# Kernel optimization log

Measured on AMD Instinct MI355X. Metric: run time of the kernel, lower is better.

The kernel has to match this reference:

```python
import jax, jax.numpy as jnp
import numpy as np

N, D, OUT, K = 1_000_000, 128, 128, 10
B2 = 4096            # final batch of nodes
B1 = B2 * K          # depth-1 frontier size


def setup_inputs() -> dict:
    key = jax.random.key(0)
    k1, k2, k3, k4, k5, k6, k7 = jax.random.split(key, 7)
    raw_features = jax.random.normal(k1, (N, D), dtype=jnp.float32)
    # SageLayer weights: [out, 2*in] (gcn=False => concat(self, agg))
    W1 = jax.random.normal(k2, (OUT, 2 * D), dtype=jnp.float32) * 0.05
    W2 = jax.random.normal(k3, (OUT, 2 * OUT), dtype=jnp.float32) * 0.05
    # depth-1 frontier node ids and their K sampled neighbors (global ids)
    nodes1 = jax.random.randint(k4, (B1,), 0, N)
    neigh1 = jax.random.randint(k5, (B1, K), 0, N)
    # batch nodes remapped to local indices into the depth-1 hidden table
    nodes2 = jax.random.randint(k6, (B2,), 0, B1)
    neigh2 = jax.random.randint(k7, (B2, K), 0, B1)
    return {"raw_features": raw_features, "W1": W1, "W2": W2,
            "nodes1": nodes1, "neigh1": neigh1,
            "nodes2": nodes2, "neigh2": neigh2}


def sage_layer(self_feats, agg_feats, W):
    # relu(concat(self, agg) @ W^T), matching SageLayer with gcn=False
    combined = jnp.concatenate([self_feats, agg_feats], axis=1)
    return jax.nn.relu(combined @ W.T)


def reference(raw_features, W1, W2, nodes1, neigh1, nodes2, neigh2):
    # Layer 1: mean-aggregate sampled neighbor raw features (gather + mean
    # replaces the dense mask.mm mean in the original).
    agg1 = jnp.mean(raw_features[neigh1], axis=1)      # [B1, D]
    h1 = sage_layer(raw_features[nodes1], agg1, W1)    # [B1, OUT]
    # Layer 2: neighbors indexed locally into the layer-1 hidden table
    agg2 = jnp.mean(h1[neigh2], axis=1)                # [B2, OUT]
    h2 = sage_layer(h1[nodes2], agg2, W2)              # [B2, OUT]
    return h2
```

## Files before the change

kernel.cpp:

```cpp
#include <hip/hip_runtime.h>


typedef __attribute__((ext_vector_type(8))) short  short8;
typedef __attribute__((ext_vector_type(8))) __bf16 bf16x8;
typedef __attribute__((ext_vector_type(4))) float  f32x4;

#define K_NEIGH 10
#define NB      32
#define PITCH   264

__device__ inline float b2f(short s) {
    union { unsigned int u; float f; } c;
    c.u = ((unsigned int)(unsigned short)s) << 16;
    return c.f;
}
__device__ inline short f2b(float f) {
    union { float f; unsigned int u; } c; c.f = f;
    unsigned int u = c.u;
    return (short)((u + 0x7fffu + ((u >> 16) & 1u)) >> 16);
}
__device__ inline unsigned int pack2(float lo, float hi) {
    return (unsigned int)(unsigned short)f2b(lo)
         | ((unsigned int)(unsigned short)f2b(hi) << 16);
}
__device__ inline bf16x8 as_bf16x8(short8 s) {
    union { short8 s; bf16x8 b; } c; c.s = s; return c.b;
}

__global__ void detect_f32(const unsigned short* __restrict__ w, int* __restrict__ flag) {
    const int lane = threadIdx.x;
    unsigned int e = ((unsigned int)w[2 * lane] >> 7) & 0xFFu;
    unsigned long long m = __ballot(e >= 132u);
    if (lane == 0) *flag = (m != 0ull) ? 1 : 0;
}

__launch_bounds__(256, 8)
__global__ void gather_agg(const void* __restrict__ table,
                           const int*  __restrict__ nodes,
                           const int*  __restrict__ neigh,
                           short*      __restrict__ comb,
                           const int*  __restrict__ flag,
                           const int table_by_flag)
{
    const int t    = threadIdx.x;
    const int lane = t & 63;
    const int node = blockIdx.x * 4 + (t >> 6);
    const bool t32 = table_by_flag && *flag;

    const int self_id = nodes[node];
    int nid[K_NEIGH];
#pragma unroll
    for (int k = 0; k < K_NEIGH; ++k) nid[k] = neigh[node * K_NEIGH + k];

    unsigned int sp;
    float a0 = 0.f, a1 = 0.f;

    if (t32) {
        const float* base = (const float*)table;
        float2 self = *(const float2*)(base + (long)self_id * 128 + lane * 2);
        float2 v[K_NEIGH];
#pragma unroll
        for (int k = 0; k < K_NEIGH; ++k)
            v[k] = *(const float2*)(base + (long)nid[k] * 128 + lane * 2);
#pragma unroll
        for (int k = 0; k < K_NEIGH; ++k) { a0 += v[k].x; a1 += v[k].y; }
        sp = pack2(self.x, self.y);
    } else {
        const short* base = (const short*)table;
        sp = *(const unsigned int*)(base + (long)self_id * 128 + lane * 2);
        unsigned int v[K_NEIGH];
#pragma unroll
        for (int k = 0; k < K_NEIGH; ++k)
            v[k] = *(const unsigned int*)(base + (long)nid[k] * 128 + lane * 2);
#pragma unroll
        for (int k = 0; k < K_NEIGH; ++k) {
            a0 += b2f((short)(v[k] & 0xFFFFu));
            a1 += b2f((short)(v[k] >> 16));
        }
    }
    unsigned int gp = pack2(a0 * 0.1f, a1 * 0.1f);
    unsigned int* crow = (unsigned int*)(comb + (long)node * 256);
    crow[lane]      = sp;
    crow[64 + lane] = gp;
}

__launch_bounds__(256, 2)
__global__ void gemm_combined(const short* __restrict__ comb,
                              const void* __restrict__ Wv,
                              void*       __restrict__ outv,
                              const int*  __restrict__ flag,
                              const int out_by_flag)
{
    __shared__ __align__(16) short lds[NB * PITCH];
    const int t    = threadIdx.x;
    const int blk  = blockIdx.x;
    const int lane = t & 63;
    const int wave = t >> 6;
    const int n15  = lane & 15;
    const int q    = lane >> 4;
    const int f32in = *flag;
    const bool o32 = out_by_flag && f32in;

    short8 bfrag[2][8];
    if (!f32in) {
        const short* W = (const short*)Wv;
#pragma unroll
        for (int ot = 0; ot < 2; ++ot) {
            const int o = wave * 32 + ot * 16 + n15;
#pragma unroll
            for (int fk = 0; fk < 8; ++fk)
                bfrag[ot][fk] = *(const short8*)(W + o * 256 + fk * 32 + q * 8);
        }
    } else {
        const float* W = (const float*)Wv;
#pragma unroll
        for (int ot = 0; ot < 2; ++ot) {
            const int o = wave * 32 + ot * 16 + n15;
#pragma unroll
            for (int fk = 0; fk < 8; ++fk) {
                const float* p = W + o * 256 + fk * 32 + q * 8;
                f32x4 v0 = *(const f32x4*)p;
                f32x4 v1 = *(const f32x4*)(p + 4);
                short8 s;
#pragma unroll
                for (int i = 0; i < 4; ++i) { s[i] = f2b(v0[i]); s[4 + i] = f2b(v1[i]); }
                bfrag[ot][fk] = s;
            }
        }
    }

    {
        const int m   = t >> 3;
        const int col = (t & 7) * 32;
        const short* src = comb + (long)blk * (NB * 256) + m * 256 + col;
        short8 x0 = *(const short8*)(src);
        short8 x1 = *(const short8*)(src + 8);
        short8 x2 = *(const short8*)(src + 16);
        short8 x3 = *(const short8*)(src + 24);
        short* dst = lds + m * PITCH + col;
        *(short8*)(dst)      = x0;
        *(short8*)(dst + 8)  = x1;
        *(short8*)(dst + 16) = x2;
        *(short8*)(dst + 24) = x3;
    }
    __syncthreads();

    f32x4 acc[2][2] = {};
#pragma unroll
    for (int mb = 0; mb < 2; ++mb) {
        const short* arow = lds + (mb * 16 + n15) * PITCH + q * 8;
        short8 af[8];
#pragma unroll
        for (int fk = 0; fk < 8; ++fk) af[fk] = *(const short8*)(arow + fk * 32);
#pragma unroll
        for (int ot = 0; ot < 2; ++ot)
#pragma unroll
            for (int fk = 0; fk < 8; ++fk)
                acc[mb][ot] = __builtin_amdgcn_mfma_f32_16x16x32_bf16(
                    as_bf16x8(af[fk]), as_bf16x8(bfrag[ot][fk]), acc[mb][ot], 0, 0, 0);
    }

#pragma unroll
    for (int mb = 0; mb < 2; ++mb)
#pragma unroll
        for (int ot = 0; ot < 2; ++ot) {
            const int col = wave * 32 + ot * 16 + n15;
#pragma unroll
            for (int r = 0; r < 4; ++r) {
                const long row = blk * NB + mb * 16 + q * 4 + r;
                float v = acc[mb][ot][r];
                v = v > 0.f ? v : 0.f;
                if (!o32) ((short*)outv)[row * 128 + col] = f2b(v);
                else      ((float*)outv)[row * 128 + col] = v;
            }
        }
}

__launch_bounds__(256, 2)
__global__ void sage_layer(const void* __restrict__ table,
                           const void* __restrict__ Wv,
                           const int*  __restrict__ nodes,
                           const int*  __restrict__ neigh,
                           void*       __restrict__ outv,
                           const int*  __restrict__ flag,
                           const int table_by_flag, const int out_by_flag)
{
    __shared__ __align__(16) short lds[NB * PITCH];
    const int t    = threadIdx.x;
    const int blk  = blockIdx.x;
    const int lane = t & 63;
    const int wave = t >> 6;
    const int n15  = lane & 15;
    const int q    = lane >> 4;
    const int f32in = *flag;
    const bool t32 = table_by_flag && f32in;
    const bool o32 = out_by_flag && f32in;

    short8 bfrag[2][8];
    if (!f32in) {
        const short* W = (const short*)Wv;
#pragma unroll
        for (int ot = 0; ot < 2; ++ot) {
            const int o = wave * 32 + ot * 16 + n15;
#pragma unroll
            for (int fk = 0; fk < 8; ++fk)
                bfrag[ot][fk] = *(const short8*)(W + o * 256 + fk * 32 + q * 8);
        }
    } else {
        const float* W = (const float*)Wv;
#pragma unroll
        for (int ot = 0; ot < 2; ++ot) {
            const int o = wave * 32 + ot * 16 + n15;
#pragma unroll
            for (int fk = 0; fk < 8; ++fk) {
                const float* p = W + o * 256 + fk * 32 + q * 8;
                f32x4 v0 = *(const f32x4*)p;
                f32x4 v1 = *(const f32x4*)(p + 4);
                short8 s;
#pragma unroll
                for (int i = 0; i < 4; ++i) { s[i] = f2b(v0[i]); s[4 + i] = f2b(v1[i]); }
                bfrag[ot][fk] = s;
            }
        }
    }

    {
        const int m    = t >> 3;
        const int part = t & 7;
        const int gi   = blk * NB + m;
        const int self_id = nodes[gi];
        int nidv[K_NEIGH];
#pragma unroll
        for (int k = 0; k < K_NEIGH; ++k) nidv[k] = neigh[gi * K_NEIGH + k];
        short8 s0, s1;
        float a[16];
#pragma unroll
        for (int i = 0; i < 16; ++i) a[i] = 0.f;

        if (!t32) {
            const short* srow = (const short*)table + (long)self_id * 128 + part * 16;
            s0 = *(const short8*)(srow);
            s1 = *(const short8*)(srow + 8);
#pragma unroll
            for (int k = 0; k < K_NEIGH; ++k) {
                const short* nrow = (const short*)table + (long)nidv[k] * 128 + part * 16;
                short8 v0 = *(const short8*)(nrow);
                short8 v1 = *(const short8*)(nrow + 8);
#pragma unroll
                for (int i = 0; i < 8; ++i) { a[i] += b2f(v0[i]); a[8 + i] += b2f(v1[i]); }
            }
        } else {
            const float* srow = (const float*)table + (long)self_id * 128 + part * 16;
            f32x4 u0 = *(const f32x4*)(srow);
            f32x4 u1 = *(const f32x4*)(srow + 4);
            f32x4 u2 = *(const f32x4*)(srow + 8);
            f32x4 u3 = *(const f32x4*)(srow + 12);
#pragma unroll
            for (int i = 0; i < 4; ++i) {
                s0[i] = f2b(u0[i]); s0[4 + i] = f2b(u1[i]);
                s1[i] = f2b(u2[i]); s1[4 + i] = f2b(u3[i]);
            }
#pragma unroll
            for (int k = 0; k < K_NEIGH; ++k) {
                const float* nrow = (const float*)table + (long)nidv[k] * 128 + part * 16;
                f32x4 v0 = *(const f32x4*)(nrow);
                f32x4 v1 = *(const f32x4*)(nrow + 4);
                f32x4 v2 = *(const f32x4*)(nrow + 8);
                f32x4 v3 = *(const f32x4*)(nrow + 12);
#pragma unroll
                for (int i = 0; i < 4; ++i) {
                    a[i] += v0[i]; a[4 + i] += v1[i]; a[8 + i] += v2[i]; a[12 + i] += v3[i];
                }
            }
        }
        short8 g0, g1;
#pragma unroll
        for (int i = 0; i < 8; ++i) { g0[i] = f2b(a[i] * 0.1f); g1[i] = f2b(a[8 + i] * 0.1f); }
        short* dst = lds + m * PITCH + part * 16;
        *(short8*)(dst)       = s0;
        *(short8*)(dst + 8)   = s1;
        *(short8*)(dst + 128) = g0;
        *(short8*)(dst + 136) = g1;
    }
    __syncthreads();

    f32x4 acc[2][2] = {};
#pragma unroll
    for (int mb = 0; mb < 2; ++mb) {
        const short* arow = lds + (mb * 16 + n15) * PITCH + q * 8;
        short8 af[8];
#pragma unroll
        for (int fk = 0; fk < 8; ++fk) af[fk] = *(const short8*)(arow + fk * 32);
#pragma unroll
        for (int ot = 0; ot < 2; ++ot)
#pragma unroll
            for (int fk = 0; fk < 8; ++fk)
                acc[mb][ot] = __builtin_amdgcn_mfma_f32_16x16x32_bf16(
                    as_bf16x8(af[fk]), as_bf16x8(bfrag[ot][fk]), acc[mb][ot], 0, 0, 0);
    }

#pragma unroll
    for (int mb = 0; mb < 2; ++mb)
#pragma unroll
        for (int ot = 0; ot < 2; ++ot) {
            const int col = wave * 32 + ot * 16 + n15;
#pragma unroll
            for (int r = 0; r < 4; ++r) {
                const long row = blk * NB + mb * 16 + q * 4 + r;
                float v = acc[mb][ot][r];
                v = v > 0.f ? v : 0.f;
                if (!o32) ((short*)outv)[row * 128 + col] = f2b(v);
                else      ((float*)outv)[row * 128 + col] = v;
            }
        }
}

extern "C" void kernel_launch(void* const* d_in, const int* in_sizes, int n_in,
                              void* d_out, int out_size, void* d_ws, size_t ws_size,
                              hipStream_t stream) {
    const void* raw    = d_in[0];
    const void* W1     = d_in[1];
    const void* W2     = d_in[2];
    const int*  nodes1 = (const int*)d_in[3];
    const int*  neigh1 = (const int*)d_in[4];
    const int*  nodes2 = (const int*)d_in[5];
    const int*  neigh2 = (const int*)d_in[6];

    int*   flag = (int*)d_ws;
    short* h1   = (short*)((char*)d_ws + 256);
    short* comb = (short*)((char*)d_ws + 256 + 10485760);

    const int B1 = in_sizes[3];
    const int B2 = in_sizes[5];

    detect_f32<<<1, 64, 0, stream>>>((const unsigned short*)W1, flag);
    gather_agg<<<B1 / 4, 256, 0, stream>>>(raw, nodes1, neigh1, comb, flag,
                                           1);
    gemm_combined<<<B1 / NB, 256, 0, stream>>>(comb, W1, h1, flag, 0);
    sage_layer<<<B2 / NB, 256, 0, stream>>>(h1, W2, nodes2, neigh2, d_out, flag,
                                            0, 1);
}
```

Baseline: 630.8 us.

## Bucket-sort layer-1 row references before gathering raw feature rows

Adds a counting-sort pipeline (histogram, scan, scatter) that orders all self and neighbor row references by 128-row bucket. Rows are then gathered in sorted order into a staging buffer, and a separate mean kernel reads them back by position. The aim is to turn random HBM row reads of the 512 MB feature table into locality-friendly accesses. The cost is several extra launches, atomics, and writing then re-reading about 90 MB of staged rows. The old path is kept as a fallback when the workspace is too small.

```diff
diff --git a/kernel.cpp b/kernel.cpp
--- a/kernel.cpp
+++ b/kernel.cpp
@@ -8,6 +8,7 @@
 #define K_NEIGH 10
 #define NB      32
 #define PITCH   264
+#define NBUCKET 8192
 
 __device__ inline float b2f(short s) {
     union { unsigned int u; float f; } c;
@@ -32,6 +33,151 @@
     unsigned int e = ((unsigned int)w[2 * lane] >> 7) & 0xFFu;
     unsigned long long m = __ballot(e >= 132u);
     if (lane == 0) *flag = (m != 0ull) ? 1 : 0;
+}
+
+
+__global__ void hist_refs(const int* __restrict__ nodes,
+                          const int* __restrict__ neigh,
+                          const int B1, const int total,
+                          int* __restrict__ hist)
+{
+    const int r = blockIdx.x * 256 + threadIdx.x;
+    if (r < total) {
+        const int id = (r < B1) ? nodes[r] : neigh[r - B1];
+        atomicAdd(&hist[id >> 7], 1);
+    }
+}
+
+__global__ void scan8k(const int* __restrict__ hist, int* __restrict__ cursor)
+{
+    __shared__ int part[1024];
+    const int tid = threadIdx.x;
+    int v[8], run[8];
+    int s = 0;
+#pragma unroll
+    for (int i = 0; i < 8; ++i) {
+        v[i] = hist[tid * 8 + i];
+        run[i] = s;
+        s += v[i];
+    }
+    part[tid] = s;
+    __syncthreads();
+    for (int off = 1; off < 1024; off <<= 1) {
+        int x = (tid >= off) ? part[tid - off] : 0;
+        __syncthreads();
+        part[tid] += x;
+        __syncthreads();
+    }
+    const int base = part[tid] - s;
+#pragma unroll
+    for (int i = 0; i < 8; ++i)
+        cursor[tid * 8 + i] = base + run[i];
+}
+
+__global__ void scatter_refs(const int* __restrict__ nodes,
+                             const int* __restrict__ neigh,
+                             const int B1, const int total,
+                             int* __restrict__ cursor,
+                             int* __restrict__ sorted_id,
+                             int* __restrict__ pos_of)
+{
+    const int r = blockIdx.x * 256 + threadIdx.x;
+    if (r < total) {
+        const int id = (r < B1) ? nodes[r] : neigh[r - B1];
+        const int p  = atomicAdd(&cursor[id >> 7], 1);
+        sorted_id[p] = id;
+        pos_of[r]    = p;
+    }
+}
+
+__launch_bounds__(256, 8)
+__global__ void gather_rows(const void* __restrict__ table,
+                            const int*  __restrict__ sorted_id,
+                            void*       __restrict__ gath,
+                            const int*  __restrict__ flag,
+                            const int total, const int table_by_flag)
+{
+    const int  t    = threadIdx.x;
+    const int  lane = t & 63;
+    const long p0   = ((long)blockIdx.x * 4 + (t >> 6)) * 4;
+    const bool t32  = table_by_flag && *flag;
+
+    int id[4];
+#pragma unroll
+    for (int j = 0; j < 4; ++j) {
+        const long p = p0 + j;
+        id[j] = (p < total) ? sorted_id[p] : 0;
+    }
+    if (t32) {
+        const float2* src = (const float2*)table;
+        float2*       dst = (float2*)gath;
+        float2 v[4];
+#pragma unroll
+        for (int j = 0; j < 4; ++j) v[j] = src[(long)id[j] * 64 + lane];
+#pragma unroll
+        for (int j = 0; j < 4; ++j) {
+            const long p = p0 + j;
+            if (p < total) dst[p * 64 + lane] = v[j];
+        }
+    } else {
+        const unsigned int* src = (const unsigned int*)table;
+        unsigned int*       dst = (unsigned int*)gath;
+        unsigned int v[4];
+#pragma unroll
+        for (int j = 0; j < 4; ++j) v[j] = src[(long)id[j] * 64 + lane];
+#pragma unroll
+        for (int j = 0; j < 4; ++j) {
+            const long p = p0 + j;
+            if (p < total) dst[p * 64 + lane] = v[j];
+        }
+    }
+}
+
+__launch_bounds__(256, 8)
+__global__ void mean_refs(const void* __restrict__ gath,
+                          const int*  __restrict__ pos_of,
+                          short*      __restrict__ comb,
+                          const int*  __restrict__ flag,
+                          const int B1, const int table_by_flag)
+{
+    const int t    = threadIdx.x;
+    const int lane = t & 63;
+    const int n    = blockIdx.x * 4 + (t >> 6);
+    if (n >= B1) return;
+    const bool t32 = table_by_flag && *flag;
+
+    const int sp_i = pos_of[n];
+    int np[K_NEIGH];
+#pragma unroll
+    for (int k = 0; k < K_NEIGH; ++k) np[k] = pos_of[B1 + n * K_NEIGH + k];
+
+    unsigned int sp;
+    float a0 = 0.f, a1 = 0.f;
+    if (t32) {
+        const float2* g = (const float2*)gath;
+        float2 self = g[(long)sp_i * 64 + lane];
+        float2 v[K_NEIGH];
+#pragma unroll
+        for (int k = 0; k < K_NEIGH; ++k) v[k] = g[(long)np[k] * 64 + lane];
+#pragma unroll
+        for (int k = 0; k < K_NEIGH; ++k) { a0 += v[k].x; a1 += v[k].y; }
+        sp = pack2(self.x, self.y);
+    } else {
+        const unsigned int* g = (const unsigned int*)gath;
+        sp = g[(long)sp_i * 64 + lane];
+        unsigned int v[K_NEIGH];
+#pragma unroll
+        for (int k = 0; k < K_NEIGH; ++k) v[k] = g[(long)np[k] * 64 + lane];
+#pragma unroll
+        for (int k = 0; k < K_NEIGH; ++k) {
+            a0 += b2f((short)(v[k] & 0xFFFFu));
+            a1 += b2f((short)(v[k] >> 16));
+        }
+    }
+    const unsigned int gp = pack2(a0 * 0.1f, a1 * 0.1f);
+    unsigned int* crow = (unsigned int*)(comb + (long)n * 256);
+    crow[lane]      = sp;
+    crow[64 + lane] = gp;
 }
 
 __launch_bounds__(256, 8)
@@ -54,7 +200,6 @@
 
     unsigned int sp;
     float a0 = 0.f, a1 = 0.f;
-
     if (t32) {
         const float* base = (const float*)table;
         float2 self = *(const float2*)(base + (long)self_id * 128 + lane * 2);
@@ -326,16 +471,47 @@
     const int*  nodes2 = (const int*)d_in[5];
     const int*  neigh2 = (const int*)d_in[6];
 
-    int*   flag = (int*)d_ws;
-    short* h1   = (short*)((char*)d_ws + 256);
-    short* comb = (short*)((char*)d_ws + 256 + 10485760);
-
-    const int B1 = in_sizes[3];
-    const int B2 = in_sizes[5];
+    const int B1    = in_sizes[3];
+    const int B2    = in_sizes[5];
+    const int total = B1 * (1 + K_NEIGH);
+
+    char* ws = (char*)d_ws;
+    int*   flag      = (int*)ws;
+    size_t o_h1      = 256;
+    size_t o_comb    = o_h1   + (size_t)B1 * 128 * 2;
+    size_t o_hist    = o_comb + (size_t)B1 * 256 * 2;
+    size_t o_cursor  = o_hist   + (size_t)NBUCKET * 4;
+    size_t o_sid     = o_cursor + (size_t)NBUCKET * 4;
+    size_t o_pos     = o_sid    + (size_t)total * 4;
+    size_t o_gath    = o_pos    + (size_t)total * 4;
+    size_t need      = o_gath   + (size_t)total * 512;
+
+    short* h1        = (short*)(ws + o_h1);
+    short* comb      = (short*)(ws + o_comb);
+    int*   hist      = (int*)(ws + o_hist);
+    int*   cursor    = (int*)(ws + o_cursor);
+    int*   sorted_id = (int*)(ws + o_sid);
+    int*   pos_of    = (int*)(ws + o_pos);
+    void*  gath      = (void*)(ws + o_gath);
 
     detect_f32<<<1, 64, 0, stream>>>((const unsigned short*)W1, flag);
-    gather_agg<<<B1 / 4, 256, 0, stream>>>(raw, nodes1, neigh1, comb, flag,
-                                           1);
+
+    if (ws_size >= need) {
+        hipMemsetAsync(hist, 0, NBUCKET * 4, stream);
+        const int gb = (total + 255) / 256;
+        hist_refs<<<gb, 256, 0, stream>>>(nodes1, neigh1, B1, total, hist);
+        scan8k<<<1, 1024, 0, stream>>>(hist, cursor);
+        scatter_refs<<<gb, 256, 0, stream>>>(nodes1, neigh1, B1, total,
+                                             cursor, sorted_id, pos_of);
+        gather_rows<<<(total + 15) / 16, 256, 0, stream>>>(raw, sorted_id, gath,
+                                                           flag, total,
+                                                           1);
+        mean_refs<<<(B1 + 3) / 4, 256, 0, stream>>>(gath, pos_of, comb, flag, B1,
+                                                    1);
+    } else {
+        gather_agg<<<B1 / 4, 256, 0, stream>>>(raw, nodes1, neigh1, comb, flag,
+                                               1);
+    }
     gemm_combined<<<B1 / NB, 256, 0, stream>>>(comb, W1, h1, flag, 0);
     sage_layer<<<B2 / NB, 256, 0, stream>>>(h1, W2, nodes2, neigh2, d_out, flag,
                                             0, 1);
```

After: 749.5 us. 1.19x slower.
